# Optimization experiments

Hardware: AMD Instinct MI355X
Metric: run time of the kernel (lower is better)

Reference implementation:

```python
import jax, jax.numpy as jnp
import numpy as np

N, C, GD, GH, GW = 4, 12, 8, 16, 16
H, W = 1024, 1024


def setup_inputs() -> dict:
    key = jax.random.key(0)
    k1, k2 = jax.random.split(key)
    bilateral_grid = jax.random.normal(k1, (N, C, GD, GH, GW), dtype=jnp.float32)
    guidemap = jax.random.uniform(k2, (N, 1, H, W), dtype=jnp.float32)
    return {"bilateral_grid": bilateral_grid, "guidemap": guidemap}


def _bilateral_slice(grid, guide):
    # grid: [N, GH, GW, GD, C]; guide: [N, H, W] in [0, 1]
    n, gh, gw, gd, c = grid.shape
    _, h, w = guide.shape
    dt = grid.dtype
    # continuous grid coordinates (HDRNet convention)
    xs = (jnp.arange(w, dtype=dt) + 0.5) * (gw / w)          # [W]
    ys = (jnp.arange(h, dtype=dt) + 0.5) * (gh / h)          # [H]
    zs = guide * gd                                           # [N,H,W]
    fx = jnp.floor(xs - 0.5)
    fy = jnp.floor(ys - 0.5)
    fz = jnp.floor(zs - 0.5)
    nidx = jnp.arange(n)[:, None, None]                       # [N,1,1]
    out = jnp.zeros((n, h, w, c), dtype=dt)
    for dz in (0, 1):
        iz = fz + dz                                          # [N,H,W]
        wz = jnp.maximum(1.0 - jnp.abs(iz + 0.5 - zs), 0.0)   # tent weight
        cz = jnp.clip(iz, 0, gd - 1).astype(jnp.int32)
        for dy in (0, 1):
            iy = fy + dy                                      # [H]
            wy = jnp.maximum(1.0 - jnp.abs(iy + 0.5 - ys), 0.0)
            cy = jnp.clip(iy, 0, gh - 1).astype(jnp.int32)
            for dx in (0, 1):
                ix = fx + dx                                  # [W]
                wx = jnp.maximum(1.0 - jnp.abs(ix + 0.5 - xs), 0.0)
                cx = jnp.clip(ix, 0, gw - 1).astype(jnp.int32)
                # gather grid[n, cy[h], cx[w], cz[n,h,w], :] -> [N,H,W,C]
                g = grid[nidx, cy[None, :, None], cx[None, None, :], cz]
                wgt = (wy[None, :, None] * wx[None, None, :] * wz)[..., None]
                out = out + wgt * g
    return out  # [N,H,W,C]


def reference(bilateral_grid, guidemap):
    # [N,C,D,GH,GW] -> [N,GH,GW,D,C]
    grid = jnp.transpose(bilateral_grid, (0, 3, 4, 2, 1))
    guide = jnp.squeeze(guidemap, axis=1)                     # [N,H,W]
    coeffs = _bilateral_slice(grid, guide)                    # [N,H,W,C]
    return jnp.transpose(coeffs, (0, 3, 1, 2))                # [N,C,H,W]
```

## Files before the change

### kernel.cpp

```cpp
#include <hip/hip_runtime.h>


#define NN 4
#define CC 12
#define GD_ 8
#define GH_ 16
#define GW_ 16
#define HH 1024
#define WW 1024

#define ZSTR 17
#define CSTR (GD_ * ZSTR)

__global__ __launch_bounds__(256) void slice_kernel(
    const float* __restrict__ grid,
    const float* __restrict__ guide,
    float* __restrict__ out)
{
    __shared__ float r[CC * CSTR + 8];

    const int row = blockIdx.x;
    const int n   = row >> 10;
    const int y   = row & (HH - 1);
    const int tid = threadIdx.x;

    float ys = ((float)y + 0.5f) * (1.0f / 64.0f);
    float fy = floorf(ys - 0.5f);
    int   by = (int)fy;
    by = by < 0 ? 0 : (by > GH_ - 2 ? GH_ - 2 : by);
    float ty = (ys - 0.5f - fy) + (float)((int)fy - by);
    ty = ty < 0.0f ? 0.0f : (ty > 1.0f ? 1.0f : ty);
    const float wy0 = 1.0f - ty, wy1 = ty;

    const float* gbase = grid + (size_t)n * (CC * GD_ * GH_ * GW_);
    for (int idx = tid; idx < CC * GD_ * GW_; idx += 256) {
        int gx = idx & 15;
        int z  = (idx >> 4) & 7;
        int c  = idx >> 7;
        const float* gp = gbase + ((c * GD_ + z) * GH_) * GW_ + gx;
        float g0 = gp[by * GW_];
        float g1 = gp[(by + 1) * GW_];
        r[c * CSTR + z * ZSTR + gx] = wy0 * g0 + wy1 * g1;
    }
    __syncthreads();

    const float4 g4 = ((const float4*)guide)[((size_t)n * HH + y) * (WW / 4) + tid];
    float gz[4] = {g4.x, g4.y, g4.z, g4.w};

    int   off0[4];
    float w00[4], w01[4], w10[4], w11[4];
#pragma unroll
    for (int j = 0; j < 4; ++j) {
        int   x  = tid * 4 + j;
        float xs = ((float)x + 0.5f) * (1.0f / 64.0f);
        float fx = floorf(xs - 0.5f);
        int   bx = (int)fx;
        bx = bx < 0 ? 0 : (bx > GW_ - 2 ? GW_ - 2 : bx);
        float tx = (xs - 0.5f - fx) + (float)((int)fx - bx);
        tx = tx < 0.0f ? 0.0f : (tx > 1.0f ? 1.0f : tx);

        float zs = gz[j] * 8.0f;
        float fz = floorf(zs - 0.5f);
        int   bz = (int)fz;
        bz = bz < 0 ? 0 : (bz > GD_ - 2 ? GD_ - 2 : bz);
        float tz = (zs - 0.5f - fz) + (float)((int)fz - bz);
        tz = tz < 0.0f ? 0.0f : (tz > 1.0f ? 1.0f : tz);

        off0[j] = bz * ZSTR + bx;
        float tx0 = 1.0f - tx, tz0 = 1.0f - tz;
        w00[j] = tz0 * tx0;  w01[j] = tz0 * tx;
        w10[j] = tz  * tx0;  w11[j] = tz  * tx;
    }

    float4* out4 = (float4*)out;
#pragma unroll
    for (int c = 0; c < CC; ++c) {
        const float* rc = r + c * CSTR;
        float acc[4];
#pragma unroll
        for (int j = 0; j < 4; ++j) {
            const float* p0 = rc + off0[j];
            float a0 = p0[0],    a1 = p0[1];
            float b0 = p0[ZSTR], b1 = p0[ZSTR + 1];
            acc[j] = w00[j] * a0 + w01[j] * a1 + w10[j] * b0 + w11[j] * b1;
        }
        out4[(((size_t)n * CC + c) * HH + y) * (WW / 4) + tid] =
            make_float4(acc[0], acc[1], acc[2], acc[3]);
    }
}

extern "C" void kernel_launch(void* const* d_in, const int* in_sizes, int n_in,
                              void* d_out, int out_size, void* d_ws, size_t ws_size,
                              hipStream_t stream) {
    const float* grid  = (const float*)d_in[0];
    const float* guide = (const float*)d_in[1];
    float* out = (float*)d_out;
    dim3 gridDim(NN * HH);
    dim3 blockDim(256);
    hipLaunchKernelGGL(slice_kernel, gridDim, blockDim, 0, stream, grid, guide, out);
}
```

Measured before the change: 213.4 us.

## Pack 2x2 corner neighbours as float4 in LDS, use nontemporal output stores

Adds a second LDS staging pass that packs the four (z,x) corner values of each cell into one float4, so the per-pixel interpolation does a single 128-bit LDS read per channel instead of four scalar reads. The guide load is moved earlier to overlap with grid staging, and the output writes become nontemporal stores to avoid polluting cache. It costs an extra barrier and about 24KB more shared memory per block, which may reduce occupancy.

```diff
diff --git a/kernel.cpp b/kernel.cpp
--- a/kernel.cpp
+++ b/kernel.cpp
@@ -10,19 +10,26 @@
 #define WW 1024
 
 #define ZSTR 17
-#define CSTR (GD_ * ZSTR)
+#define RS_CSTR (GD_ * ZSTR)
+#define C4_GXSTR 9
+#define C4_CSTR (GW_ * C4_GXSTR)
+
+typedef float f32x4 __attribute__((ext_vector_type(4)));
 
 __global__ __launch_bounds__(256) void slice_kernel(
     const float* __restrict__ grid,
     const float* __restrict__ guide,
     float* __restrict__ out)
 {
-    __shared__ float r[CC * CSTR + 8];
+    __shared__ float  rs[CC * RS_CSTR + 8];
+    __shared__ float4 c4[CC * C4_CSTR];
 
     const int row = blockIdx.x;
     const int n   = row >> 10;
     const int y   = row & (HH - 1);
     const int tid = threadIdx.x;
+
+    const float4 g4 = ((const float4*)guide)[((size_t)n * HH + y) * (WW / 4) + tid];
 
     float ys = ((float)y + 0.5f) * (1.0f / 64.0f);
     float fy = floorf(ys - 0.5f);
@@ -40,14 +47,28 @@
         const float* gp = gbase + ((c * GD_ + z) * GH_) * GW_ + gx;
         float g0 = gp[by * GW_];
         float g1 = gp[(by + 1) * GW_];
-        r[c * CSTR + z * ZSTR + gx] = wy0 * g0 + wy1 * g1;
+        rs[c * RS_CSTR + z * ZSTR + gx] = wy0 * g0 + wy1 * g1;
     }
     __syncthreads();
 
-    const float4 g4 = ((const float4*)guide)[((size_t)n * HH + y) * (WW / 4) + tid];
+    for (int idx = tid; idx < CC * GW_ * GD_; idx += 256) {
+        int z   = idx & 7;
+        int gx  = (idx >> 3) & 15;
+        int c   = idx >> 7;
+        int z1  = z  < GD_ - 1 ? z  + 1 : z;
+        int gx1 = gx < GW_ - 1 ? gx + 1 : gx;
+        const float* rc = rs + c * RS_CSTR;
+        float v00 = rc[z  * ZSTR + gx ];
+        float v01 = rc[z  * ZSTR + gx1];
+        float v10 = rc[z1 * ZSTR + gx ];
+        float v11 = rc[z1 * ZSTR + gx1];
+        c4[c * C4_CSTR + gx * C4_GXSTR + z] = make_float4(v00, v01, v10, v11);
+    }
+    __syncthreads();
+
     float gz[4] = {g4.x, g4.y, g4.z, g4.w};
 
-    int   off0[4];
+    int   off4[4];
     float w00[4], w01[4], w10[4], w11[4];
 #pragma unroll
     for (int j = 0; j < 4; ++j) {
@@ -66,26 +87,24 @@
         float tz = (zs - 0.5f - fz) + (float)((int)fz - bz);
         tz = tz < 0.0f ? 0.0f : (tz > 1.0f ? 1.0f : tz);
 
-        off0[j] = bz * ZSTR + bx;
+        off4[j] = bx * C4_GXSTR + bz;
         float tx0 = 1.0f - tx, tz0 = 1.0f - tz;
         w00[j] = tz0 * tx0;  w01[j] = tz0 * tx;
         w10[j] = tz  * tx0;  w11[j] = tz  * tx;
     }
 
-    float4* out4 = (float4*)out;
+    f32x4* out4 = (f32x4*)out;
 #pragma unroll
     for (int c = 0; c < CC; ++c) {
-        const float* rc = r + c * CSTR;
         float acc[4];
 #pragma unroll
         for (int j = 0; j < 4; ++j) {
-            const float* p0 = rc + off0[j];
-            float a0 = p0[0],    a1 = p0[1];
-            float b0 = p0[ZSTR], b1 = p0[ZSTR + 1];
-            acc[j] = w00[j] * a0 + w01[j] * a1 + w10[j] * b0 + w11[j] * b1;
+            float4 v = c4[c * C4_CSTR + off4[j]];
+            acc[j] = w00[j] * v.x + w01[j] * v.y + w10[j] * v.z + w11[j] * v.w;
         }
-        out4[(((size_t)n * CC + c) * HH + y) * (WW / 4) + tid] =
-            make_float4(acc[0], acc[1], acc[2], acc[3]);
+        f32x4 o = {acc[0], acc[1], acc[2], acc[3]};
+        __builtin_nontemporal_store(
+            o, &out4[(((size_t)n * CC + c) * HH + y) * (WW / 4) + tid]);
     }
 }
 
```

Result: slower. 225.8 us (+5.8%).
